# Performance work log

Measured on AMD Instinct MI355X. Metric: run time of the kernel, lower is better.

Reference implementation:

```python
import jax, jax.numpy as jnp
import numpy as np

D_MODEL = 1024
N_HEADS = 16
HEAD_DIM = D_MODEL // N_HEADS
B, L = 2, 2048


def setup_inputs() -> dict:
    key = jax.random.key(0)
    ks = jax.random.split(key, 11)
    s = 1.0 / np.sqrt(D_MODEL)
    inp = {
        'query': jax.random.normal(ks[0], (B, L, D_MODEL), dtype=jnp.float32),
        'key': jax.random.normal(ks[1], (B, L, D_MODEL), dtype=jnp.float32),
        'value': jax.random.normal(ks[2], (B, L, D_MODEL), dtype=jnp.float32),
        'Wq_w': jax.random.normal(ks[3], (D_MODEL, D_MODEL), dtype=jnp.float32) * s,
        'Wq_b': jnp.zeros((D_MODEL,), dtype=jnp.float32),
        'Wk_w': jax.random.normal(ks[4], (D_MODEL, D_MODEL), dtype=jnp.float32) * s,
        'Wk_b': jnp.zeros((D_MODEL,), dtype=jnp.float32),
        'Wv_w': jax.random.normal(ks[5], (D_MODEL, D_MODEL), dtype=jnp.float32) * s,
        'Wv_b': jnp.zeros((D_MODEL,), dtype=jnp.float32),
        'Wo_w': jax.random.normal(ks[6], (D_MODEL, D_MODEL), dtype=jnp.float32) * s,
        'Wo_b': jnp.zeros((D_MODEL,), dtype=jnp.float32),
    }
    return inp


def reference(query, key, value, Wq_w, Wq_b, Wk_w, Wk_b, Wv_w, Wv_b, Wo_w, Wo_b):
    b = query.shape[0]
    # torch Linear: y = x @ W^T + b
    Q = query @ Wq_w.T + Wq_b
    K = key @ Wk_w.T + Wk_b
    V = value @ Wv_w.T + Wv_b
    # [B, L, D] -> [B, H, L, hd]
    def split_heads(x):
        return x.reshape(b, -1, N_HEADS, HEAD_DIM).transpose(0, 2, 1, 3)
    Qh, Kh, Vh = split_heads(Q), split_heads(K), split_heads(V)
    scale = 1.0 / jnp.sqrt(jnp.float32(HEAD_DIM))
    # energy: [B, H, Lq, Lk]
    energy = jnp.einsum('bhqd,bhkd->bhqk', Qh, Kh) * scale
    # NOTE: original code applies softmax over dim=1 (the HEADS axis) — faithful reproduction
    attn = jax.nn.softmax(energy, axis=1)
    out = jnp.einsum('bhqk,bhkd->bhqd', attn, Vh)  # [B, H, Lq, hd]
    out = out.transpose(0, 2, 1, 3).reshape(b, -1, D_MODEL)
    return out @ Wo_w.T + Wo_b
```

## Files before the change

### kernel.cpp

```cpp
#include <hip/hip_runtime.h>
#include <hip/hip_bf16.h>
#include <hip/hip_fp16.h>

#define DM 1024
#define NH 16
#define HD 64
#define LL 2048

typedef __attribute__((ext_vector_type(8))) short bf16x8;
typedef __attribute__((ext_vector_type(4))) float f32x4;

#define MFMA16(a,b,c) __builtin_amdgcn_mfma_f32_16x16x32_bf16((a),(b),(c),0,0,0)

#define GL16(g, l) __builtin_amdgcn_global_load_lds( \
    (const __attribute__((address_space(1))) unsigned int*)(g), \
    (__attribute__((address_space(3))) unsigned int*)(l), 16, 0, 0)

__device__ __forceinline__ ushort f2bf(float f) {
  union { float f; unsigned int u; } v; v.f = f;
  unsigned int u = v.u + 0x7fffu + ((v.u >> 16) & 1u);
  return (ushort)(u >> 16);
}

__global__ __launch_bounds__(256) void cvt6(const float* __restrict__ s0, ushort* __restrict__ d0, int n0,
                                            const float* __restrict__ s1, ushort* __restrict__ d1, int n1,
                                            const float* __restrict__ s2, ushort* __restrict__ d2, int n2,
                                            const float* __restrict__ s3, ushort* __restrict__ d3, int n3,
                                            const float* __restrict__ s4, ushort* __restrict__ d4, int n4,
                                            const float* __restrict__ s5, ushort* __restrict__ d5, int n5) {
  int i = (blockIdx.x * 256 + threadIdx.x) * 4;
  const float* s; ushort* d;
  if (i < n0) { s = s0; d = d0; }
  else if ((i -= n0) < n1) { s = s1; d = d1; }
  else if ((i -= n1) < n2) { s = s2; d = d2; }
  else if ((i -= n2) < n3) { s = s3; d = d3; }
  else if ((i -= n3) < n4) { s = s4; d = d4; }
  else if ((i -= n4) < n5) { s = s5; d = d5; }
  else return;
  float4 v = *(const float4*)(s + i);
  union { ushort u[4]; unsigned long long ll; } o;
  o.u[0] = f2bf(v.x); o.u[1] = f2bf(v.y); o.u[2] = f2bf(v.z); o.u[3] = f2bf(v.w);
  *(unsigned long long*)(d + i) = o.ll;
}

__global__ __launch_bounds__(256) void gemm_qkv(const ushort* __restrict__ qA, const ushort* __restrict__ qW,
                                                const float* __restrict__ qb, ushort* __restrict__ qO,
                                                const ushort* __restrict__ kA, const ushort* __restrict__ kW,
                                                const float* __restrict__ kb, ushort* __restrict__ kO,
                                                const ushort* __restrict__ vA, const ushort* __restrict__ vW,
                                                const float* __restrict__ vb, ushort* __restrict__ vO) {
  __shared__ ushort lA[2][128][64];
  __shared__ ushort lB[2][128][64];
  const int z = blockIdx.z;
  const ushort* Ab; const ushort* Wb; const float* bias; ushort* outp;
  float alpha; bool trans;
  if (z == 0)      { Ab = qA; Wb = qW; bias = qb; outp = qO; alpha = 0.125f; trans = false; }
  else if (z == 1) { Ab = kA; Wb = kW; bias = kb; outp = kO; alpha = 1.0f;   trans = false; }
  else             { Ab = vA; Wb = vW; bias = vb; outp = vO; alpha = 1.0f;   trans = true;  }

  const int m0 = blockIdx.x * 128, n0 = blockIdx.y * 128;
  const int t = threadIdx.x;
  const int w = t >> 6, lane = t & 63, lr = lane & 15, lg = lane >> 4;
  const int wm = (w >> 1) * 64, wn = (w & 1) * 64;
  const int lrow8 = lane >> 3;
  const int scol = ((lane & 7) ^ lrow8) * 8;

  f32x4 acc[4][4];
  #pragma unroll
  for (int i = 0; i < 4; ++i)
    #pragma unroll
    for (int j = 0; j < 4; ++j) acc[i][j] = (f32x4){0.f, 0.f, 0.f, 0.f};

  #pragma unroll
  for (int c = 0; c < 4; ++c) {
    GL16(Ab + (m0 + w * 32 + c * 8 + lrow8) * DM + scol, &lA[0][w * 32 + c * 8][0]);
    GL16(Wb + (n0 + w * 32 + c * 8 + lrow8) * DM + scol, &lB[0][w * 32 + c * 8][0]);
  }
  __syncthreads();

  int cur = 0;
  for (int k0 = 0; k0 < DM; k0 += 64) {
    if (k0 + 64 < DM) {
      #pragma unroll
      for (int c = 0; c < 4; ++c) {
        GL16(Ab + (m0 + w * 32 + c * 8 + lrow8) * DM + k0 + 64 + scol, &lA[cur ^ 1][w * 32 + c * 8][0]);
        GL16(Wb + (n0 + w * 32 + c * 8 + lrow8) * DM + k0 + 64 + scol, &lB[cur ^ 1][w * 32 + c * 8][0]);
      }
    }
    #pragma unroll
    for (int ks = 0; ks < 2; ++ks) {
      bf16x8 aF[4], bF[4];
      #pragma unroll
      for (int i = 0; i < 4; ++i)
        aF[i] = *(const bf16x8*)&lA[cur][wm + i * 16 + lr][(((ks * 4 + lg) ^ (lr & 7)) * 8)];
      #pragma unroll
      for (int j = 0; j < 4; ++j)
        bF[j] = *(const bf16x8*)&lB[cur][wn + j * 16 + lr][(((ks * 4 + lg) ^ (lr & 7)) * 8)];
      #pragma unroll
      for (int i = 0; i < 4; ++i)
        #pragma unroll
        for (int j = 0; j < 4; ++j)
          acc[i][j] = MFMA16(aF[i], bF[j], acc[i][j]);
    }
    __syncthreads();
    cur ^= 1;
  }

  #pragma unroll
  for (int i = 0; i < 4; ++i)
    #pragma unroll
    for (int j = 0; j < 4; ++j)
      #pragma unroll
      for (int r = 0; r < 4; ++r) {
        int m = m0 + wm + i * 16 + lg * 4 + r;
        int n = n0 + wn + j * 16 + lr;
        float v = (acc[i][j][r] + bias[n]) * alpha;
        int b = m >> 11, q = m & 2047, h = n >> 6, d = n & 63;
        if (!trans)
          outp[((b * NH + h) * LL + q) * HD + d] = f2bf(v);
        else
          outp[((b * NH + h) * HD + d) * LL + q] = f2bf(v);
      }
}

__global__ __launch_bounds__(256) void gemm_out(const ushort* __restrict__ Ab,
                                                const ushort* __restrict__ Wb,
                                                const float* __restrict__ bias,
                                                float* __restrict__ outf) {
  __shared__ ushort lA[2][128][64];
  __shared__ ushort lB[2][128][64];
  const int m0 = blockIdx.x * 128, n0 = blockIdx.y * 128;
  const int t = threadIdx.x;
  const int w = t >> 6, lane = t & 63, lr = lane & 15, lg = lane >> 4;
  const int wm = (w >> 1) * 64, wn = (w & 1) * 64;
  const int lrow8 = lane >> 3;
  const int scol = ((lane & 7) ^ lrow8) * 8;

  f32x4 acc[4][4];
  #pragma unroll
  for (int i = 0; i < 4; ++i)
    #pragma unroll
    for (int j = 0; j < 4; ++j) acc[i][j] = (f32x4){0.f, 0.f, 0.f, 0.f};

  #pragma unroll
  for (int c = 0; c < 4; ++c) {
    GL16(Ab + (m0 + w * 32 + c * 8 + lrow8) * DM + scol, &lA[0][w * 32 + c * 8][0]);
    GL16(Wb + (n0 + w * 32 + c * 8 + lrow8) * DM + scol, &lB[0][w * 32 + c * 8][0]);
  }
  __syncthreads();

  int cur = 0;
  for (int k0 = 0; k0 < DM; k0 += 64) {
    if (k0 + 64 < DM) {
      #pragma unroll
      for (int c = 0; c < 4; ++c) {
        GL16(Ab + (m0 + w * 32 + c * 8 + lrow8) * DM + k0 + 64 + scol, &lA[cur ^ 1][w * 32 + c * 8][0]);
        GL16(Wb + (n0 + w * 32 + c * 8 + lrow8) * DM + k0 + 64 + scol, &lB[cur ^ 1][w * 32 + c * 8][0]);
      }
    }
    #pragma unroll
    for (int ks = 0; ks < 2; ++ks) {
      bf16x8 aF[4], bF[4];
      #pragma unroll
      for (int i = 0; i < 4; ++i)
        aF[i] = *(const bf16x8*)&lA[cur][wm + i * 16 + lr][(((ks * 4 + lg) ^ (lr & 7)) * 8)];
      #pragma unroll
      for (int j = 0; j < 4; ++j)
        bF[j] = *(const bf16x8*)&lB[cur][wn + j * 16 + lr][(((ks * 4 + lg) ^ (lr & 7)) * 8)];
      #pragma unroll
      for (int i = 0; i < 4; ++i)
        #pragma unroll
        for (int j = 0; j < 4; ++j)
          acc[i][j] = MFMA16(aF[i], bF[j], acc[i][j]);
    }
    __syncthreads();
    cur ^= 1;
  }

  #pragma unroll
  for (int i = 0; i < 4; ++i)
    #pragma unroll
    for (int j = 0; j < 4; ++j)
      #pragma unroll
      for (int r = 0; r < 4; ++r) {
        int m = m0 + wm + i * 16 + lg * 4 + r;
        int n = n0 + wn + j * 16 + lr;
        outf[m * DM + n] = acc[i][j][r] + bias[n];
      }
}

__global__ __launch_bounds__(256) void pass_a_m(const ushort* __restrict__ Qh,
                                                const ushort* __restrict__ Kh,
                                                __half* __restrict__ rdenH) {
  __shared__ ushort lQ[2][128][64];
  __shared__ ushort lK[2][128][64];
  const int b = blockIdx.z, q0 = blockIdx.y * 128, k0 = blockIdx.x * 128;
  const int t = threadIdx.x, w = t >> 6, lane = t & 63, lr = lane & 15, lg = lane >> 4;
  const int lrow8 = lane >> 3;
  const int scol = ((lane & 7) ^ lrow8) * 8;

  f32x4 acc[2][8];
  #pragma unroll
  for (int i = 0; i < 2; ++i)
    #pragma unroll
    for (int j = 0; j < 8; ++j) acc[i][j] = (f32x4){0.f, 0.f, 0.f, 0.f};

  #pragma unroll
  for (int c = 0; c < 4; ++c) {
    GL16(Qh + ((b * NH) * LL + q0 + w * 32 + c * 8 + lrow8) * HD + scol, &lQ[0][w * 32 + c * 8][0]);
    GL16(Kh + ((b * NH) * LL + k0 + w * 32 + c * 8 + lrow8) * HD + scol, &lK[0][w * 32 + c * 8][0]);
  }
  __syncthreads();

  int cur = 0;
  for (int h = 0; h < NH; ++h) {
    if (h + 1 < NH) {
      #pragma unroll
      for (int c = 0; c < 4; ++c) {
        GL16(Qh + ((b * NH + h + 1) * LL + q0 + w * 32 + c * 8 + lrow8) * HD + scol, &lQ[cur ^ 1][w * 32 + c * 8][0]);
        GL16(Kh + ((b * NH + h + 1) * LL + k0 + w * 32 + c * 8 + lrow8) * HD + scol, &lK[cur ^ 1][w * 32 + c * 8][0]);
      }
    }
    #pragma unroll
    for (int i = 0; i < 2; ++i) {
      int qrow = w * 32 + i * 16 + lr;
      bf16x8 a0 = *(const bf16x8*)&lQ[cur][qrow][((lg ^ (lr & 7)) * 8)];
      bf16x8 a1 = *(const bf16x8*)&lQ[cur][qrow][(((4 + lg) ^ (lr & 7)) * 8)];
      #pragma unroll
      for (int j = 0; j < 8; ++j) {
        int krow = j * 16 + lr;
        bf16x8 b0 = *(const bf16x8*)&lK[cur][krow][((lg ^ (lr & 7)) * 8)];
        bf16x8 b1 = *(const bf16x8*)&lK[cur][krow][(((4 + lg) ^ (lr & 7)) * 8)];
        f32x4 e = {0.f, 0.f, 0.f, 0.f};
        e = MFMA16(b0, a0, e);
        e = MFMA16(b1, a1, e);
        #pragma unroll
        for (int r = 0; r < 4; ++r) acc[i][j][r] += __expf(e[r]);
      }
    }
    __syncthreads();
    cur ^= 1;
  }

  #pragma unroll
  for (int i = 0; i < 2; ++i)
    #pragma unroll
    for (int j = 0; j < 8; ++j) {
      int q = q0 + w * 32 + i * 16 + lr;
      int k = k0 + j * 16 + lg * 4;
      union { __half2 h2[2]; uint2 u; } pk;
      pk.h2[0] = __floats2half2_rn(__builtin_amdgcn_rcpf(acc[i][j][0]),
                                   __builtin_amdgcn_rcpf(acc[i][j][1]));
      pk.h2[1] = __floats2half2_rn(__builtin_amdgcn_rcpf(acc[i][j][2]),
                                   __builtin_amdgcn_rcpf(acc[i][j][3]));
      *(uint2*)&rdenH[(size_t)(b * LL + q) * LL + k] = pk.u;
    }
}

#define PB_BODY(T, SC, SL, BR, BL)                                             \
  {                                                                            \
    if ((T) + 2 < 32) {                                                        \
      GL16(Kh + (bh * LL + ((T) + 2) * 64 + w * 8 + lrow8) * HD + scol,        \
           &lK[BL][w * 8][0]);                                                 \
      GL16(Vt + (bh * HD + w * 8 + lrow8) * LL + ((T) + 2) * 64 + scol,        \
           &lV[BL][w * 8][0]);                                                 \
      _Pragma("unroll")                                                        \
      for (int j = 0; j < 4; ++j)                                              \
        SL[j] = *(const uint2*)(rrow + ((T) + 2) * 64 + j * 16 + lg * 4);      \
    }                                                                          \
    __builtin_amdgcn_s_setprio(1);                                             \
    if ((T) > 0) {                                                             \
      bf16x8 aP0 = *(const bf16x8*)&U.p[w][lr][lg * 8];                        \
      bf16x8 aP1 = *(const bf16x8*)&U.p[w][lr][32 + lg * 8];                   \
      _Pragma("unroll")                                                        \
      for (int j = 0; j < 4; ++j) {                                            \
        accO[j] = MFMA16(aP0, vF0[j], accO[j]);                                \
        accO[j] = MFMA16(aP1, vF1[j], accO[j]);                                \
      }                                                                        \
    }                                                                          \
    f32x4 e[4];                                                                \
    _Pragma("unroll")                                                          \
    for (int j = 0; j < 4; ++j) {                                              \
      int krow = j * 16 + lr;                                                  \
      bf16x8 kf0 = *(const bf16x8*)&lK[BR][krow][((lg ^ (lr & 7)) * 8)];       \
      bf16x8 kf1 = *(const bf16x8*)&lK[BR][krow][(((4 + lg) ^ (lr & 7)) * 8)]; \
      e[j] = (f32x4){0.f, 0.f, 0.f, 0.f};                                      \
      e[j] = MFMA16(kf0, aQ0, e[j]);                                           \
      e[j] = MFMA16(kf1, aQ1, e[j]);                                           \
    }                                                                          \
    __builtin_amdgcn_s_setprio(0);                                             \
    _Pragma("unroll")                                                          \
    for (int j = 0; j < 4; ++j) {                                              \
      int vrow = j * 16 + lr;                                                  \
      vF0[j] = *(const bf16x8*)&lV[BR][vrow][((lg ^ (lr & 7)) * 8)];           \
      vF1[j] = *(const bf16x8*)&lV[BR][vrow][(((4 + lg) ^ (lr & 7)) * 8)];     \
    }                                                                          \
    _Pragma("unroll")                                                          \
    for (int j = 0; j < 4; ++j) {                                              \
      float2 f0 = __half22float2(*reinterpret_cast<const __half2*>(&SC[j].x)); \
      float2 f1 = __half22float2(*reinterpret_cast<const __half2*>(&SC[j].y)); \
      union { __hip_bfloat162 b2[2]; uint2 u; } pk;                            \
      pk.b2[0] = __float22bfloat162_rn(make_float2(__expf(e[j][0]) * f0.x,     \
                                                   __expf(e[j][1]) * f0.y));   \
      pk.b2[1] = __float22bfloat162_rn(make_float2(__expf(e[j][2]) * f1.x,     \
                                                   __expf(e[j][3]) * f1.y));   \
      *(uint2*)&U.p[w][lr][j * 16 + lg * 4] = pk.u;                            \
    }                                                                          \
    if ((T) < 31) {                                                            \
      if ((T) + 2 < 32) { asm volatile("s_waitcnt vmcnt(6)" ::: "memory"); }   \
      else              { asm volatile("s_waitcnt vmcnt(0)" ::: "memory"); }   \
      __builtin_amdgcn_sched_barrier(0);                                       \
      __builtin_amdgcn_s_barrier();                                            \
      __builtin_amdgcn_sched_barrier(0);                                       \
    }                                                                          \
  }

__global__ __launch_bounds__(512, 4) void pass_b_m(const ushort* __restrict__ Qh,
                                                   const ushort* __restrict__ Kh,
                                                   const ushort* __restrict__ Vt,
                                                   const __half* __restrict__ rdenH,
                                                   ushort* __restrict__ AO) {
  __shared__ union UQP { ushort q[128][64]; ushort p[8][16][72]; } U;
  __shared__ ushort lK[3][64][64];
  __shared__ ushort lV[3][64][64];
  const int q0 = blockIdx.x * 128, h = blockIdx.y, b = blockIdx.z;
  const int t = threadIdx.x, w = t >> 6, lane = t & 63, lr = lane & 15, lg = lane >> 4;
  const int lrow8 = lane >> 3;
  const int scol = ((lane & 7) ^ lrow8) * 8;
  const int bh = b * NH + h;

  #pragma unroll
  for (int u = 0; u < 2; ++u) {
    int c = u * 512 + t;
    int row = c >> 3, col = (c & 7) * 8;
    *(bf16x8*)&U.q[row][col] = *(const bf16x8*)&Qh[(bh * LL + q0 + row) * HD + col];
  }
  GL16(Kh + (bh * LL + w * 8 + lrow8) * HD + scol, &lK[0][w * 8][0]);
  GL16(Vt + (bh * HD + w * 8 + lrow8) * LL + scol, &lV[0][w * 8][0]);
  GL16(Kh + (bh * LL + 64 + w * 8 + lrow8) * HD + scol, &lK[1][w * 8][0]);
  GL16(Vt + (bh * HD + w * 8 + lrow8) * LL + 64 + scol, &lV[1][w * 8][0]);
  const int qg = q0 + w * 16 + lr;
  const __half* rrow = rdenH + (size_t)(b * LL + qg) * LL;
  uint2 rA[4], rB[4], rC2[4];
  #pragma unroll
  for (int j = 0; j < 4; ++j) {
    rA[j] = *(const uint2*)(rrow + j * 16 + lg * 4);
    rB[j] = *(const uint2*)(rrow + 64 + j * 16 + lg * 4);
  }
  __syncthreads();

  bf16x8 aQ0 = *(const bf16x8*)&U.q[w * 16 + lr][lg * 8];
  bf16x8 aQ1 = *(const bf16x8*)&U.q[w * 16 + lr][32 + lg * 8];
  __syncthreads();

  f32x4 accO[4];
  #pragma unroll
  for (int j = 0; j < 4; ++j) accO[j] = (f32x4){0.f, 0.f, 0.f, 0.f};
  bf16x8 vF0[4], vF1[4];

  for (int tt = 0; tt < 30; tt += 3) {
    PB_BODY(tt + 0, rA, rC2, 0, 2)
    PB_BODY(tt + 1, rB, rA, 1, 0)
    PB_BODY(tt + 2, rC2, rB, 2, 1)
  }
  PB_BODY(30, rA, rC2, 0, 2)
  PB_BODY(31, rB, rA, 1, 0)

  {
    bf16x8 aP0 = *(const bf16x8*)&U.p[w][lr][lg * 8];
    bf16x8 aP1 = *(const bf16x8*)&U.p[w][lr][32 + lg * 8];
    #pragma unroll
    for (int j = 0; j < 4; ++j) {
      accO[j] = MFMA16(aP0, vF0[j], accO[j]);
      accO[j] = MFMA16(aP1, vF1[j], accO[j]);
    }
  }

  #pragma unroll
  for (int j = 0; j < 4; ++j)
    #pragma unroll
    for (int r = 0; r < 4; ++r) {
      int q = q0 + w * 16 + lg * 4 + r;
      int d = j * 16 + lr;
      AO[(b * LL + q) * DM + h * HD + d] = f2bf(accO[j][r]);
    }
}

extern "C" void kernel_launch(void* const* d_in, const int* in_sizes, int n_in,
                              void* d_out, int out_size, void* d_ws, size_t ws_size,
                              hipStream_t stream) {
  const float* query = (const float*)d_in[0];
  const float* key   = (const float*)d_in[1];
  const float* value = (const float*)d_in[2];
  const float* Wq_w  = (const float*)d_in[3];
  const float* Wq_b  = (const float*)d_in[4];
  const float* Wk_w  = (const float*)d_in[5];
  const float* Wk_b  = (const float*)d_in[6];
  const float* Wv_w  = (const float*)d_in[7];
  const float* Wv_b  = (const float*)d_in[8];
  const float* Wo_w  = (const float*)d_in[9];
  const float* Wo_b  = (const float*)d_in[10];

  char* ws = (char*)d_ws;
  char* dob = (char*)d_out;
  ushort* Qh  = (ushort*)(ws);
  ushort* Kh  = (ushort*)(ws + (8u  << 20));
  ushort* Vt  = (ushort*)(ws + (16u << 20));
  ushort* AO  = (ushort*)(ws + (24u << 20));
  ushort* qbf = (ushort*)(ws + (32u << 20));
  ushort* kbf = (ushort*)(ws + (40u << 20));
  ushort* Wob = (ushort*)(ws + (32u << 20));
  ushort* vbf = (ushort*)(dob);
  ushort* Wqb = (ushort*)(dob + (8u  << 20));
  ushort* Wkb = (ushort*)(dob + (10u << 20));
  ushort* Wvb = (ushort*)(dob + (12u << 20));
  __half* rdn = (__half*)d_out;

  const int NA = 2 * LL * DM;
  const int NW = DM * DM;

  cvt6<<<(3 * NA + 3 * NW) / 1024, 256, 0, stream>>>(
      query, qbf, NA, key, kbf, NA, value, vbf, NA,
      Wq_w, Wqb, NW, Wk_w, Wkb, NW, Wv_w, Wvb, NW);

  gemm_qkv<<<dim3(32, 8, 3), 256, 0, stream>>>(qbf, Wqb, Wq_b, Qh,
                                               kbf, Wkb, Wk_b, Kh,
                                               vbf, Wvb, Wv_b, Vt);

  cvt6<<<NW / 1024, 256, 0, stream>>>(Wo_w, Wob, NW,
                                      nullptr, nullptr, 0, nullptr, nullptr, 0,
                                      nullptr, nullptr, 0, nullptr, nullptr, 0,
                                      nullptr, nullptr, 0);

  pass_a_m<<<dim3(16, 16, 2), 256, 0, stream>>>(Qh, Kh, rdn);
  pass_b_m<<<dim3(16, NH, 2), 512, 0, stream>>>(Qh, Kh, Vt, rdn, AO);

  gemm_out<<<dim3(32, 8), 256, 0, stream>>>(AO, Wob, Wo_b, (float*)d_out);
}
```

Baseline: 197.1 us.

## Load V fragments straight into registers and shrink attention blocks to 64 queries

The second attention pass no longer stages V tiles in LDS. Each wave loads its V MFMA fragments from global memory into registers one tile ahead, alternating between two register sets. The K LDS ring drops from triple to double buffering with a plain __syncthreads. Blocks shrink from 512 to 256 threads covering 64 queries, with twice as many blocks launched, to cut LDS use and raise occupancy. In exchange, every wave fetches the whole V tile on its own, which adds redundant global/L2 traffic, and the prefetch pipeline is one stage shorter.

```diff
diff --git a/kernel.cpp b/kernel.cpp
--- a/kernel.cpp
+++ b/kernel.cpp
@@ -257,16 +257,17 @@
     }
 }
 
-#define PB_BODY(T, SC, SL, BR, BL)                                             \
+#define PB_BODY(T, RC, RN, VX0, VX1)                                           \
   {                                                                            \
-    if ((T) + 2 < 32) {                                                        \
-      GL16(Kh + (bh * LL + ((T) + 2) * 64 + w * 8 + lrow8) * HD + scol,        \
-           &lK[BL][w * 8][0]);                                                 \
-      GL16(Vt + (bh * HD + w * 8 + lrow8) * LL + ((T) + 2) * 64 + scol,        \
-           &lV[BL][w * 8][0]);                                                 \
+    const int k0 = (T) * 64;                                                   \
+    if ((T) + 1 < 32) {                                                        \
+      _Pragma("unroll")                                                        \
+      for (int c = 0; c < 2; ++c)                                              \
+        GL16(Kh + (bh * LL + k0 + 64 + w * 16 + c * 8 + lrow8) * HD + scol,    \
+             &lK[((T) + 1) & 1][w * 16 + c * 8][0]);                           \
       _Pragma("unroll")                                                        \
       for (int j = 0; j < 4; ++j)                                              \
-        SL[j] = *(const uint2*)(rrow + ((T) + 2) * 64 + j * 16 + lg * 4);      \
+        RN[j] = *(const uint2*)(rrow + k0 + 64 + j * 16 + lg * 4);             \
     }                                                                          \
     __builtin_amdgcn_s_setprio(1);                                             \
     if ((T) > 0) {                                                             \
@@ -274,16 +275,24 @@
       bf16x8 aP1 = *(const bf16x8*)&U.p[w][lr][32 + lg * 8];                   \
       _Pragma("unroll")                                                        \
       for (int j = 0; j < 4; ++j) {                                            \
-        accO[j] = MFMA16(aP0, vF0[j], accO[j]);                                \
-        accO[j] = MFMA16(aP1, vF1[j], accO[j]);                                \
+        accO[j] = MFMA16(aP0, VX0[j], accO[j]);                                \
+        accO[j] = MFMA16(aP1, VX1[j], accO[j]);                                \
+      }                                                                        \
+    }                                                                          \
+    if ((T) + 1 < 32) {                                                        \
+      _Pragma("unroll")                                                        \
+      for (int j = 0; j < 4; ++j) {                                            \
+        const ushort* vp = Vt + (size_t)(bh * HD + j * 16 + lr) * LL + k0 + 64;\
+        VX0[j] = *(const bf16x8*)(vp + lg * 8);                                \
+        VX1[j] = *(const bf16x8*)(vp + 32 + lg * 8);                           \
       }                                                                        \
     }                                                                          \
     f32x4 e[4];                                                                \
     _Pragma("unroll")                                                          \
     for (int j = 0; j < 4; ++j) {                                              \
       int krow = j * 16 + lr;                                                  \
-      bf16x8 kf0 = *(const bf16x8*)&lK[BR][krow][((lg ^ (lr & 7)) * 8)];       \
-      bf16x8 kf1 = *(const bf16x8*)&lK[BR][krow][(((4 + lg) ^ (lr & 7)) * 8)]; \
+      bf16x8 kf0 = *(const bf16x8*)&lK[(T) & 1][krow][((lg ^ (lr & 7)) * 8)];  \
+      bf16x8 kf1 = *(const bf16x8*)&lK[(T) & 1][krow][(((4 + lg) ^ (lr & 7)) * 8)]; \
       e[j] = (f32x4){0.f, 0.f, 0.f, 0.f};                                      \
       e[j] = MFMA16(kf0, aQ0, e[j]);                                           \
       e[j] = MFMA16(kf1, aQ1, e[j]);                                           \
@@ -291,14 +300,8 @@
     __builtin_amdgcn_s_setprio(0);                                             \
     _Pragma("unroll")                                                          \
     for (int j = 0; j < 4; ++j) {                                              \
-      int vrow = j * 16 + lr;                                                  \
-      vF0[j] = *(const bf16x8*)&lV[BR][vrow][((lg ^ (lr & 7)) * 8)];           \
-      vF1[j] = *(const bf16x8*)&lV[BR][vrow][(((4 + lg) ^ (lr & 7)) * 8)];     \
-    }                                                                          \
-    _Pragma("unroll")                                                          \
-    for (int j = 0; j < 4; ++j) {                                              \
-      float2 f0 = __half22float2(*reinterpret_cast<const __half2*>(&SC[j].x)); \
-      float2 f1 = __half22float2(*reinterpret_cast<const __half2*>(&SC[j].y)); \
+      float2 f0 = __half22float2(*reinterpret_cast<const __half2*>(&RC[j].x)); \
+      float2 f1 = __half22float2(*reinterpret_cast<const __half2*>(&RC[j].y)); \
       union { __hip_bfloat162 b2[2]; uint2 u; } pk;                            \
       pk.b2[0] = __float22bfloat162_rn(make_float2(__expf(e[j][0]) * f0.x,     \
                                                    __expf(e[j][1]) * f0.y));   \
@@ -306,24 +309,17 @@
                                                    __expf(e[j][3]) * f1.y));   \
       *(uint2*)&U.p[w][lr][j * 16 + lg * 4] = pk.u;                            \
     }                                                                          \
-    if ((T) < 31) {                                                            \
-      if ((T) + 2 < 32) { asm volatile("s_waitcnt vmcnt(6)" ::: "memory"); }   \
-      else              { asm volatile("s_waitcnt vmcnt(0)" ::: "memory"); }   \
-      __builtin_amdgcn_sched_barrier(0);                                       \
-      __builtin_amdgcn_s_barrier();                                            \
-      __builtin_amdgcn_sched_barrier(0);                                       \
-    }                                                                          \
-  }
-
-__global__ __launch_bounds__(512, 4) void pass_b_m(const ushort* __restrict__ Qh,
+    if ((T) < 31) __syncthreads();                                             \
+  }
+
+__global__ __launch_bounds__(256, 4) void pass_b_m(const ushort* __restrict__ Qh,
                                                    const ushort* __restrict__ Kh,
                                                    const ushort* __restrict__ Vt,
                                                    const __half* __restrict__ rdenH,
                                                    ushort* __restrict__ AO) {
-  __shared__ union UQP { ushort q[128][64]; ushort p[8][16][72]; } U;
-  __shared__ ushort lK[3][64][64];
-  __shared__ ushort lV[3][64][64];
-  const int q0 = blockIdx.x * 128, h = blockIdx.y, b = blockIdx.z;
+  __shared__ union UQP { ushort q[64][64]; ushort p[4][16][72]; } U;
+  __shared__ ushort lK[2][64][64];
+  const int q0 = blockIdx.x * 64, h = blockIdx.y, b = blockIdx.z;
   const int t = threadIdx.x, w = t >> 6, lane = t & 63, lr = lane & 15, lg = lane >> 4;
   const int lrow8 = lane >> 3;
   const int scol = ((lane & 7) ^ lrow8) * 8;
@@ -331,22 +327,25 @@
 
   #pragma unroll
   for (int u = 0; u < 2; ++u) {
-    int c = u * 512 + t;
+    int c = u * 256 + t;
     int row = c >> 3, col = (c & 7) * 8;
     *(bf16x8*)&U.q[row][col] = *(const bf16x8*)&Qh[(bh * LL + q0 + row) * HD + col];
   }
-  GL16(Kh + (bh * LL + w * 8 + lrow8) * HD + scol, &lK[0][w * 8][0]);
-  GL16(Vt + (bh * HD + w * 8 + lrow8) * LL + scol, &lV[0][w * 8][0]);
-  GL16(Kh + (bh * LL + 64 + w * 8 + lrow8) * HD + scol, &lK[1][w * 8][0]);
-  GL16(Vt + (bh * HD + w * 8 + lrow8) * LL + 64 + scol, &lV[1][w * 8][0]);
+  #pragma unroll
+  for (int c = 0; c < 2; ++c)
+    GL16(Kh + (bh * LL + w * 16 + c * 8 + lrow8) * HD + scol, &lK[0][w * 16 + c * 8][0]);
+  bf16x8 vA0[4], vA1[4], vB0[4], vB1[4];
+  #pragma unroll
+  for (int j = 0; j < 4; ++j) {
+    const ushort* vp = Vt + (size_t)(bh * HD + j * 16 + lr) * LL;
+    vA0[j] = *(const bf16x8*)(vp + lg * 8);
+    vA1[j] = *(const bf16x8*)(vp + 32 + lg * 8);
+  }
   const int qg = q0 + w * 16 + lr;
   const __half* rrow = rdenH + (size_t)(b * LL + qg) * LL;
-  uint2 rA[4], rB[4], rC2[4];
-  #pragma unroll
-  for (int j = 0; j < 4; ++j) {
-    rA[j] = *(const uint2*)(rrow + j * 16 + lg * 4);
-    rB[j] = *(const uint2*)(rrow + 64 + j * 16 + lg * 4);
-  }
+  uint2 rA[4], rB[4];
+  #pragma unroll
+  for (int j = 0; j < 4; ++j) rA[j] = *(const uint2*)(rrow + j * 16 + lg * 4);
   __syncthreads();
 
   bf16x8 aQ0 = *(const bf16x8*)&U.q[w * 16 + lr][lg * 8];
@@ -356,23 +355,19 @@
   f32x4 accO[4];
   #pragma unroll
   for (int j = 0; j < 4; ++j) accO[j] = (f32x4){0.f, 0.f, 0.f, 0.f};
-  bf16x8 vF0[4], vF1[4];
-
-  for (int tt = 0; tt < 30; tt += 3) {
-    PB_BODY(tt + 0, rA, rC2, 0, 2)
-    PB_BODY(tt + 1, rB, rA, 1, 0)
-    PB_BODY(tt + 2, rC2, rB, 2, 1)
-  }
-  PB_BODY(30, rA, rC2, 0, 2)
-  PB_BODY(31, rB, rA, 1, 0)
+
+  for (int tt = 0; tt < 32; tt += 2) {
+    PB_BODY(tt + 0, rA, rB, vB0, vB1)
+    PB_BODY(tt + 1, rB, rA, vA0, vA1)
+  }
 
   {
     bf16x8 aP0 = *(const bf16x8*)&U.p[w][lr][lg * 8];
     bf16x8 aP1 = *(const bf16x8*)&U.p[w][lr][32 + lg * 8];
     #pragma unroll
     for (int j = 0; j < 4; ++j) {
-      accO[j] = MFMA16(aP0, vF0[j], accO[j]);
-      accO[j] = MFMA16(aP1, vF1[j], accO[j]);
+      accO[j] = MFMA16(aP0, vB0[j], accO[j]);
+      accO[j] = MFMA16(aP1, vB1[j], accO[j]);
     }
   }
 
@@ -433,7 +428,7 @@
                                       nullptr, nullptr, 0);
 
   pass_a_m<<<dim3(16, 16, 2), 256, 0, stream>>>(Qh, Kh, rdn);
-  pass_b_m<<<dim3(16, NH, 2), 512, 0, stream>>>(Qh, Kh, Vt, rdn, AO);
+  pass_b_m<<<dim3(32, NH, 2), 256, 0, stream>>>(Qh, Kh, Vt, rdn, AO);
 
   gemm_out<<<dim3(32, 8), 256, 0, stream>>>(AO, Wob, Wo_b, (float*)d_out);
 }
```

New measurement: 352.8 us. +79.0%, slower.
